# Performance work log

Measured on AMD Instinct MI355X. Metric: run time of the kernel, lower is better.

## Reference

```python
import jax, jax.numpy as jnp
import numpy as np

NT, NS, NH, NG, NR, NC = 365, 300, 128, 32, 8, 1


def _linear_params(key, fin, fout):
    k1, k2 = jax.random.split(key)
    s = 1.0 / np.sqrt(fin)
    W = jax.random.uniform(k1, (fout, fin), minval=-s, maxval=s, dtype=jnp.float32)
    b = jax.random.uniform(k2, (fout,), minval=-s, maxval=s, dtype=jnp.float32)
    return W, b


def setup_inputs() -> dict:
    key = jax.random.key(0)
    ks = jax.random.split(key, 9)
    x = jax.random.normal(ks[0], (NT, NS, 6), dtype=jnp.float32)
    xc = jax.random.normal(ks[1], (NS, NG), dtype=jnp.float32)
    fcR_w1, fcR_b1 = _linear_params(ks[2], NG, 256)
    fcR_w2, fcR_b2 = _linear_params(ks[3], 256, NH * NR)
    fcW_w1, fcW_b1 = _linear_params(ks[4], NG, 256)
    fcW_w2, fcW_b2 = _linear_params(ks[5], 256, NH * 7)
    fcT_w1, fcT_b1 = _linear_params(ks[6], 6 + NG, 256)
    fcT_w2, fcT_b2 = _linear_params(ks[7], 256, NH * 3)
    fcCT_w, fcCT_b = _linear_params(ks[8], 2 + NG, NC * NH * 3)
    return dict(x=x, xc=xc,
                fcR_w1=fcR_w1, fcR_b1=fcR_b1, fcR_w2=fcR_w2, fcR_b2=fcR_b2,
                fcW_w1=fcW_w1, fcW_b1=fcW_b1, fcW_w2=fcW_w2, fcW_b2=fcW_b2,
                fcT_w1=fcT_w1, fcT_b1=fcT_b1, fcT_w2=fcT_w2, fcT_b2=fcT_b2,
                fcCT_w=fcCT_w, fcCT_b=fcCT_b)


def _mlp(x, w1, b1, w2, b2):
    # Linear -> Tanh -> Dropout(identity in eval) -> Linear
    h = jnp.tanh(x @ w1.T + b1)
    return h @ w2.T + b2


def _conv_ts(q, r):
    # q: [nt, ns, nh]; r: [ns, nh, nr] routing weights. Causal temporal conv:
    # out[t] = sum_i q[t-i] * r[..., i]  (zero padded on the left)
    nt = q.shape[0]
    nr = r.shape[-1]
    qp = jnp.concatenate([jnp.zeros((nr - 1,) + q.shape[1:], q.dtype), q], axis=0)
    out = qp[nr - 1: nr - 1 + nt] * r[None, :, :, 0]
    for i in range(1, nr):
        out = out + qp[nr - 1 - i: nr - 1 - i + nt] * r[None, :, :, i]
    return out


def reference(x, xc, fcR_w1, fcR_b1, fcR_w2, fcR_b2,
              fcW_w1, fcW_b1, fcW_w2, fcW_b2,
              fcT_w1, fcT_b1, fcT_w2, fcT_b2,
              fcCT_w, fcCT_b):
    nh, nr = NH, NR
    P, E, T1, T2 = x[..., 0], x[..., 1], x[..., 2], x[..., 3]
    nt, ns = P.shape
    xcT = jnp.broadcast_to(xc[None], (nt, ns, xc.shape[-1]))
    xT = jnp.concatenate([x, xcT], axis=-1)                      # [nt, ns, 6+ng]

    # static gates per (site, bucket): sepPar with ['sigmoid']*4,'exp','relu','skip'
    w = _mlp(xc, fcW_w1, fcW_b1, fcW_w2, fcW_b2)                 # [ns, nh*7]
    kp = jax.nn.sigmoid(w[:, 0 * nh:1 * nh])
    ks_ = jax.nn.sigmoid(w[:, 1 * nh:2 * nh])
    kg = jax.nn.sigmoid(w[:, 2 * nh:3 * nh])
    gp = jax.nn.sigmoid(w[:, 3 * nh:4 * nh])
    gL = jnp.exp(w[:, 4 * nh:5 * nh]) * 2.0
    qb = jax.nn.relu(w[:, 5 * nh:6 * nh])
    ga = jax.nn.softmax(w[:, 6 * nh:7 * nh], axis=1)             # [ns, nh]

    # time-varying gates: ['skip','relu','exp']; vi overridden by hardsigmoid(v*2)
    v = _mlp(xT, fcT_w1, fcT_b1, fcT_w2, fcT_b2)                 # [nt, ns, nh*3]
    vi = jnp.clip(v[:, :, :nh] * 2.0 / 6.0 + 0.5, 0.0, 1.0)     # F.hardsigmoid(v*2)
    ve = jax.nn.relu(v[:, :, nh:2 * nh]) * 2.0
    vm = jnp.exp(v[:, :, 2 * nh:3 * nh])

    wR = _mlp(xc, fcR_w1, fcR_b1, fcR_w2, fcR_b2)                # [ns, nh*nr]
    r = jax.nn.relu(wR[:, :nh * nr]).reshape(ns, nh, nr)

    # snow fraction vf = arccos((T1+T2)/(T2-T1))/3.1415, overridden at extremes
    denom = T2 - T1
    ratio = jnp.clip((T1 + T2) / jnp.where(denom == 0, 1.0, denom), -1.0, 1.0)
    vf = jnp.arccos(ratio) / 3.1415
    vf = jnp.where(T1 >= 0, 0.0, jnp.where(T2 <= 0, 1.0, vf))
    Ps = P * vf                                                  # snow  [nt, ns]
    Pl = (P * (1.0 - vf))[:, :, None] * vi                       # rain  [nt, ns, nh]
    Ev = E[:, :, None] * ve                                      # evap  [nt, ns, nh]

    def step(carry, inp):
        Sf, Ss, Sg = carry
        Ps_k, Pl_k, Ev_k, vm_k = inp
        qf = jnp.minimum(Sf + Ps_k, vm_k)
        Sf = jax.nn.relu(Sf + Ps_k - vm_k)
        H = jax.nn.relu(Ss + Pl_k + qf - Ev_k)
        qp_ = jax.nn.relu(kp * (H - gL))
        qs = ks_ * jnp.minimum(H, gL)
        Ss = H - qp_ - qs
        qso = qs * (1.0 - gp)
        qsg = qs * gp
        qg = kg * (Sg + qsg) + qb
        Sg = (1.0 - kg) * (Sg + qsg) - qb
        return (Sf, Ss, Sg), (qp_, qso, qg)

    z = jnp.zeros((ns, nh), dtype=x.dtype)
    _, (Q1T, Q2T, Q3T) = jax.lax.scan(step, (z, z, z),
                                      (Ps[:, :, None], Pl, Ev, vm))

    Q1R = _conv_ts(Q1T, r)
    Q2R = _conv_ts(Q2T, r)
    Q3R = _conv_ts(Q3T, r)
    outQ = jnp.sum((Q1R + Q2R + Q3R) * ga, axis=2)               # [nt, ns]

    xTc = jnp.concatenate([T1[:, :, None], T2[:, :, None], xcT], axis=-1)
    wC = xTc @ fcCT_w.T + fcCT_b                                 # [nt, ns, nh*3]
    cp = jnp.exp(wC[:, :, 0 * nh:1 * nh])
    cs = jnp.exp(wC[:, :, 1 * nh:2 * nh])
    cg = jnp.exp(wC[:, :, 2 * nh:3 * nh])
    C1R = _conv_ts(Q1T * cp / 10.0, r)
    C2R = _conv_ts(Q2T * cs, r)
    C3R = _conv_ts(Q3T * cg, r)
    outC = jnp.sum((C1R + C2R + C3R) * ga, axis=2) / outQ
    return outQ, outC
```

## Files before the change

### kernel.cpp

```cpp
#include <hip/hip_runtime.h>
#include <math.h>

#define NTT 365
#define NSS 300
#define NROWS (NTT*NSS)
#define TPAD 384

using bf16x8 = __attribute__((ext_vector_type(8))) short;
using f32x4  = __attribute__((ext_vector_type(4))) float;

__device__ __forceinline__ float sigf(float v) { return 1.0f / (1.0f + __expf(-v)); }

__device__ __forceinline__ float tanhfast(float x) {
    float e = __expf(2.0f * x);
    return 1.0f - 2.0f * __builtin_amdgcn_rcpf(1.0f + e);
}

__device__ __forceinline__ unsigned short f2bf(float f) {
    unsigned u = __builtin_bit_cast(unsigned, f);
    u += 0x7FFFu + ((u >> 16) & 1u);
    return (unsigned short)(u >> 16);
}

__global__ __launch_bounds__(256) void k_prep(const float* __restrict__ w1,
                                              const float* __restrict__ w2,
                                              unsigned short* __restrict__ w1bf,
                                              unsigned short* __restrict__ w2bf)
{
    int idx = blockIdx.x * 256 + threadIdx.x;
    if (idx < 256 * 64) {
        int k = idx & 63;
        int r = idx >> 6;
        w1bf[idx] = (k < 38) ? f2bf(w1[r * 38 + k]) : (unsigned short)0;
    }
    int idx2 = idx - 256 * 64;
    if (idx2 >= 0 && idx2 < 384 * 256) w2bf[idx2] = f2bf(w2[idx2]);
}

__global__ __launch_bounds__(256) void k_site(
    const float* __restrict__ xc,
    const float* __restrict__ wW1, const float* __restrict__ bW1,
    const float* __restrict__ wW2, const float* __restrict__ bW2,
    const float* __restrict__ wR1, const float* __restrict__ bR1,
    const float* __restrict__ wR2, const float* __restrict__ bR2,
    float* __restrict__ wsite, float* __restrict__ rsite)
{
    __shared__ float xcb[10][32];
    __shared__ float hW[10][256];
    __shared__ float hR[10][256];
    int tid = threadIdx.x;
    int s0 = blockIdx.x * 10;
    int os = blockIdx.y;
    for (int i = tid; i < 10 * 32; i += 256) xcb[i / 32][i % 32] = xc[s0 * 32 + i];
    __syncthreads();
    {
        int j = tid;
        float aW[10], aR[10];
#pragma unroll
        for (int r = 0; r < 10; ++r) { aW[r] = bW1[j]; aR[r] = bR1[j]; }
        for (int k = 0; k < 32; ++k) {
            float wv = wW1[j * 32 + k], rv = wR1[j * 32 + k];
#pragma unroll
            for (int r = 0; r < 10; ++r) { float xv = xcb[r][k]; aW[r] += xv * wv; aR[r] += xv * rv; }
        }
#pragma unroll
        for (int r = 0; r < 10; ++r) { hW[r][j] = tanhfast(aW[r]); hR[r][j] = tanhfast(aR[r]); }
    }
    __syncthreads();
    if (tid < 240) {
        int o_lin = os * 240 + tid;
        float acc[10];
        if (o_lin < 896) {
            int o = o_lin;
#pragma unroll
            for (int r = 0; r < 10; ++r) acc[r] = bW2[o];
            for (int k = 0; k < 256; ++k) {
                float wv = wW2[o * 256 + k];
#pragma unroll
                for (int r = 0; r < 10; ++r) acc[r] += hW[r][k] * wv;
            }
#pragma unroll
            for (int r = 0; r < 10; ++r) wsite[(s0 + r) * 896 + o] = acc[r];
        } else {
            int o = o_lin - 896;
#pragma unroll
            for (int r = 0; r < 10; ++r) acc[r] = bR2[o];
            for (int k = 0; k < 256; ++k) {
                float wv = wR2[o * 256 + k];
#pragma unroll
                for (int r = 0; r < 10; ++r) acc[r] += hR[r][k] * wv;
            }
#pragma unroll
            for (int r = 0; r < 10; ++r) rsite[(s0 + r) * 1024 + o] = acc[r];
        }
    }
}

__global__ __launch_bounds__(128) void k_softmax_ga(const float* __restrict__ wsite,
                                                    float* __restrict__ ga)
{
    int s = blockIdx.x, tid = threadIdx.x;
    __shared__ float red[2];
    float v = wsite[s * 896 + 6 * 128 + tid];
    float m = v;
#pragma unroll
    for (int off = 32; off >= 1; off >>= 1) m = fmaxf(m, __shfl_xor(m, off));
    if ((tid & 63) == 0) red[tid >> 6] = m;
    __syncthreads();
    m = fmaxf(red[0], red[1]);
    __syncthreads();
    float e = __expf(v - m);
    float ssum = e;
#pragma unroll
    for (int off = 32; off >= 1; off >>= 1) ssum += __shfl_xor(ssum, off);
    if ((tid & 63) == 0) red[tid >> 6] = ssum;
    __syncthreads();
    ssum = red[0] + red[1];
    ga[s * 128 + tid] = e / ssum;
}

__global__ __launch_bounds__(512) void k_fcT(
    const float* __restrict__ x, const float* __restrict__ xc,
    const unsigned short* __restrict__ w1bf, const float* __restrict__ b1,
    const unsigned short* __restrict__ w2bf, const float* __restrict__ b2,
    float4* __restrict__ PT, float2* __restrict__ NV)
{
    __shared__ unsigned short A1[64][72];
    __shared__ unsigned short hb[64][264];
    __shared__ float2 pfE[64];
    int tid = threadIdx.x;
    int row0 = blockIdx.x * 64;

    for (int idx = tid; idx < 64 * 64; idx += 512) {
        int r = idx >> 6, c = idx & 63;
        int g = row0 + r;
        float val = 0.0f;
        if (g < NROWS) {
            if (c < 6) val = x[g * 6 + c];
            else if (c < 38) { int s = g % NSS; val = xc[s * 32 + (c - 6)]; }
        }
        A1[r][c] = f2bf(val);
    }
    if (tid < 64) {
        int r = tid, g = row0 + r;
        float P = 0, E = 0, T1 = 0, T2 = 0;
        if (g < NROWS) { P = x[g * 6]; E = x[g * 6 + 1]; T1 = x[g * 6 + 2]; T2 = x[g * 6 + 3]; }
        float den = T2 - T1;
        float dg = (den == 0.0f) ? 1.0f : den;
        float ratio = fminf(fmaxf((T1 + T2) / dg, -1.0f), 1.0f);
        float vf = acosf(ratio) * (1.0f / 3.1415f);
        vf = (T1 >= 0.0f) ? 0.0f : ((T2 <= 0.0f) ? 1.0f : vf);
        pfE[r] = make_float2(P * (1.0f - vf), 2.0f * E);
        if (g < NROWS) PT[g] = make_float4(P * vf, T1, T2, vf);
    }
    __syncthreads();

    int lane = tid & 63, wv = tid >> 6;
    int r16 = lane & 15;
    int kg = (lane >> 4) * 8;
    int rq = (lane >> 4) * 4;

    {
        int mt = wv & 3, nb = (wv >> 2) * 8;
        f32x4 acc[8];
#pragma unroll
        for (int i = 0; i < 8; ++i) acc[i] = (f32x4){0.f, 0.f, 0.f, 0.f};
#pragma unroll
        for (int ks = 0; ks < 2; ++ks) {
            bf16x8 a = *(const bf16x8*)&A1[mt * 16 + r16][ks * 32 + kg];
#pragma unroll
            for (int i = 0; i < 8; ++i) {
                bf16x8 b = *(const bf16x8*)(w1bf + ((nb + i) * 16 + r16) * 64 + ks * 32 + kg);
                acc[i] = __builtin_amdgcn_mfma_f32_16x16x32_bf16(a, b, acc[i], 0, 0, 0);
            }
        }
#pragma unroll
        for (int i = 0; i < 8; ++i) {
            int col = (nb + i) * 16 + r16;
            float bias = b1[col];
#pragma unroll
            for (int j = 0; j < 4; ++j) {
                int row = mt * 16 + rq + j;
                hb[row][col] = f2bf(tanhfast(acc[i][j] + bias));
            }
        }
    }
    __syncthreads();

    {
        int cb0 = wv * 16, cb1 = 128 + wv * 16, cb2 = 256 + wv * 16;
        f32x4 acc[4][3];
#pragma unroll
        for (int m = 0; m < 4; ++m)
#pragma unroll
            for (int c = 0; c < 3; ++c) acc[m][c] = (f32x4){0.f, 0.f, 0.f, 0.f};
#pragma unroll
        for (int ks = 0; ks < 8; ++ks) {
            bf16x8 b0 = *(const bf16x8*)(w2bf + (cb0 + r16) * 256 + ks * 32 + kg);
            bf16x8 b1v = *(const bf16x8*)(w2bf + (cb1 + r16) * 256 + ks * 32 + kg);
            bf16x8 b2v = *(const bf16x8*)(w2bf + (cb2 + r16) * 256 + ks * 32 + kg);
#pragma unroll
            for (int m = 0; m < 4; ++m) {
                bf16x8 a = *(const bf16x8*)&hb[m * 16 + r16][ks * 32 + kg];
                acc[m][0] = __builtin_amdgcn_mfma_f32_16x16x32_bf16(a, b0, acc[m][0], 0, 0, 0);
                acc[m][1] = __builtin_amdgcn_mfma_f32_16x16x32_bf16(a, b1v, acc[m][1], 0, 0, 0);
                acc[m][2] = __builtin_amdgcn_mfma_f32_16x16x32_bf16(a, b2v, acc[m][2], 0, 0, 0);
            }
        }
        int hcol = cb0 + r16;
        float bias0 = b2[cb0 + r16], bias1 = b2[cb1 + r16], bias2 = b2[cb2 + r16];
#pragma unroll
        for (int m = 0; m < 4; ++m) {
            float2 pf[4];
#pragma unroll
            for (int j = 0; j < 4; ++j) pf[j] = pfE[m * 16 + rq + j];
#pragma unroll
            for (int j = 0; j < 4; ++j) {
                int r = m * 16 + rq + j;
                int g = row0 + r;
                if (g < NROWS) {
                    float vi = fminf(fmaxf((acc[m][0][j] + bias0) * (1.0f / 3.0f) + 0.5f, 0.0f), 1.0f);
                    float pl = pf[j].x * vi;
                    float ev = pf[j].y * fmaxf(acc[m][1][j] + bias1, 0.0f);
                    float vmv = __expf(acc[m][2][j] + bias2);
                    NV[(size_t)g * 128 + hcol] = make_float2(pl - ev, vmv);
                }
            }
        }
    }
}

__global__ __launch_bounds__(64) void k_scan(
    const float* __restrict__ xc,
    const float* __restrict__ wsite, const float* __restrict__ rsite,
    const float* __restrict__ gaw,
    const float* __restrict__ ctw, const float* __restrict__ ctb,
    const float4* __restrict__ PTg, const float2* __restrict__ NV,
    float* __restrict__ pQ, float* __restrict__ pC)
{
    __shared__ float4 ptlds[TPAD];
    __shared__ __align__(16) float red[16][68];
    int lane = threadIdx.x;
    int b = blockIdx.x;
    int s = b >> 1, half = b & 1;
    int h = half * 64 + lane;

    for (int t = lane; t < TPAD; t += 64) ptlds[t] = PTg[(size_t)t * NSS + s];

    const float* wrow = wsite + s * 896;
    float kp = sigf(wrow[0 * 128 + h]);
    float ks = sigf(wrow[1 * 128 + h]);
    float kg = sigf(wrow[2 * 128 + h]);
    float gp = sigf(wrow[3 * 128 + h]);
    float gpc = 1.0f - gp;
    float gL = __expf(wrow[4 * 128 + h]) * 2.0f;
    float kpgl = kp * gL;
    float qb = fmaxf(wrow[5 * 128 + h], 0.0f);
    float ga = gaw[s * 128 + h];
    float rt0 = fmaxf(rsite[s * 1024 + h * 8 + 0], 0.0f) * ga;
    float rt1 = fmaxf(rsite[s * 1024 + h * 8 + 1], 0.0f) * ga;
    float rt2 = fmaxf(rsite[s * 1024 + h * 8 + 2], 0.0f) * ga;
    float rt3 = fmaxf(rsite[s * 1024 + h * 8 + 3], 0.0f) * ga;
    float rt4 = fmaxf(rsite[s * 1024 + h * 8 + 4], 0.0f) * ga;
    float rt5 = fmaxf(rsite[s * 1024 + h * 8 + 5], 0.0f) * ga;
    float rt6 = fmaxf(rsite[s * 1024 + h * 8 + 6], 0.0f) * ga;
    float rt7 = fmaxf(rsite[s * 1024 + h * 8 + 7], 0.0f) * ga;
    const float L2E = 1.4426950408889634f;
    const float LG01 = -3.3219280948873623f;
    float cpw0, cpw1, cpb, csw0, csw1, csb, cgw0, cgw1, cgb;
    {
        const float* wr = ctw + (0 * 128 + h) * 34;
        float base = ctb[0 * 128 + h];
        for (int k = 0; k < 32; ++k) base += wr[2 + k] * xc[s * 32 + k];
        cpw0 = wr[0] * L2E; cpw1 = wr[1] * L2E; cpb = base * L2E + LG01;
    }
    {
        const float* wr = ctw + (1 * 128 + h) * 34;
        float base = ctb[1 * 128 + h];
        for (int k = 0; k < 32; ++k) base += wr[2 + k] * xc[s * 32 + k];
        csw0 = wr[0] * L2E; csw1 = wr[1] * L2E; csb = base * L2E;
    }
    {
        const float* wr = ctw + (2 * 128 + h) * 34;
        float base = ctb[2 * 128 + h];
        for (int k = 0; k < 32; ++k) base += wr[2 + k] * xc[s * 32 + k];
        cgw0 = wr[0] * L2E; cgw1 = wr[1] * L2E; cgb = base * L2E;
    }
    float Sf = 0.0f, Ss = 0.0f, Sg = 0.0f;
    float q0 = 0, q1 = 0, q2 = 0, q3 = 0, q4 = 0, q5 = 0, q6 = 0, q7 = 0;
    float c0 = 0, c1 = 0, c2 = 0, c3 = 0, c4 = 0, c5 = 0, c6 = 0, c7 = 0;

    const float2* nvbase = NV + (size_t)s * 128 + h;
    float2 nv[16];
#pragma unroll
    for (int i = 0; i < 16; ++i) nv[i] = nvbase[(size_t)i * NSS * 128];

    float4 ptc = ptlds[0];
    float4 ptn = ptlds[1];

    auto reduce8 = [&](int base) {
        int v = lane >> 2, sub = lane & 3;
        const float4* rp = (const float4*)&red[v][0];
        float4 a0 = rp[sub * 4 + 0];
        float4 a1 = rp[sub * 4 + 1];
        float4 a2 = rp[sub * 4 + 2];
        float4 a3 = rp[sub * 4 + 3];
        float sA = (a0.x + a0.y) + (a0.z + a0.w);
        float sB = (a1.x + a1.y) + (a1.z + a1.w);
        float sC = (a2.x + a2.y) + (a2.z + a2.w);
        float sD = (a3.x + a3.y) + (a3.z + a3.w);
        float sm = (sA + sB) + (sC + sD);
        sm += __shfl_xor(sm, 1);
        sm += __shfl_xor(sm, 2);
        int t = base + (v & 7);
        if (sub == 0 && t < NTT) {
            float* bp = (v < 8) ? pQ : pC;
            bp[((size_t)t * NSS + s) * 2 + half] = sm;
        }
    };

    for (int tb = 0; tb < 368; tb += 16) {
#pragma unroll
        for (int u = 0; u < 16; ++u) {
            int t = tb + u;
            float net = nv[u].x, vm = nv[u].y;
            nv[u] = nvbase[(size_t)(t + 16) * NSS * 128];
            float psv = ptc.x, T1 = ptc.y, T2 = ptc.z;
            ptc = ptn;
            ptn = ptlds[t + 2];
            float t1v = Sf + psv;
            float qf = fminf(t1v, vm);
            Sf = fmaxf(t1v - vm, 0.0f);
            float H = fmaxf(Ss + qf + net, 0.0f);
            float qp = fmaxf(kp * H - kpgl, 0.0f);
            float qs = ks * fminf(H, gL);
            Ss = H - qp - qs;
            float qso = qs * gpc;
            float qsg = qs * gp;
            float tg = Sg + qsg;
            float qg = kg * tg + qb;
            Sg = tg - qg;
            float cp = exp2f(cpw0 * T1 + cpw1 * T2 + cpb);
            float cs = exp2f(csw0 * T1 + csw1 * T2 + csb);
            float cg = exp2f(cgw0 * T1 + cgw1 * T2 + cgb);
            float QS = qp + qso + qg;
            float CS = qp * cp + qso * cs + qg * cg;
            q0 += QS * rt0; q1 += QS * rt1; q2 += QS * rt2; q3 += QS * rt3;
            q4 += QS * rt4; q5 += QS * rt5; q6 += QS * rt6; q7 += QS * rt7;
            c0 += CS * rt0; c1 += CS * rt1; c2 += CS * rt2; c3 += CS * rt3;
            c4 += CS * rt4; c5 += CS * rt5; c6 += CS * rt6; c7 += CS * rt7;
            red[u & 7][lane] = q0;
            red[8 + (u & 7)][lane] = c0;
            q0 = q1; q1 = q2; q2 = q3; q3 = q4; q4 = q5; q5 = q6; q6 = q7; q7 = 0.0f;
            c0 = c1; c1 = c2; c2 = c3; c3 = c4; c4 = c5; c5 = c6; c6 = c7; c7 = 0.0f;
            if (u == 7) reduce8(tb);
            if (u == 15) reduce8(tb + 8);
        }
    }
}

__global__ __launch_bounds__(256) void k_final(const float* __restrict__ pQ,
                                               const float* __restrict__ pC,
                                               float* __restrict__ out)
{
    int i = blockIdx.x * 256 + threadIdx.x;
    if (i < NROWS) {
        float q = pQ[i * 2] + pQ[i * 2 + 1];
        float c = pC[i * 2] + pC[i * 2 + 1];
        out[i] = q;
        out[NROWS + i] = c / q;
    }
}

extern "C" void kernel_launch(void* const* d_in, const int* in_sizes, int n_in,
                              void* d_out, int out_size, void* d_ws, size_t ws_size,
                              hipStream_t stream)
{
    const float* x      = (const float*)d_in[0];
    const float* xc     = (const float*)d_in[1];
    const float* fcR_w1 = (const float*)d_in[2];
    const float* fcR_b1 = (const float*)d_in[3];
    const float* fcR_w2 = (const float*)d_in[4];
    const float* fcR_b2 = (const float*)d_in[5];
    const float* fcW_w1 = (const float*)d_in[6];
    const float* fcW_b1 = (const float*)d_in[7];
    const float* fcW_w2 = (const float*)d_in[8];
    const float* fcW_b2 = (const float*)d_in[9];
    const float* fcT_w1 = (const float*)d_in[10];
    const float* fcT_b1 = (const float*)d_in[11];
    const float* fcT_w2 = (const float*)d_in[12];
    const float* fcT_b2 = (const float*)d_in[13];
    const float* fcCT_w = (const float*)d_in[14];
    const float* fcCT_b = (const float*)d_in[15];
    float* out = (float*)d_out;

    float* ws = (float*)d_ws;
    size_t o_w    = 0;
    size_t o_r    = o_w  + 300 * 896;
    size_t o_ga   = o_r  + 300 * 1024;
    size_t o_PT   = o_ga + 300 * 128;
    size_t o_NV   = o_PT + (size_t)TPAD * NSS * 4;
    size_t o_pQ   = o_NV + (size_t)TPAD * NSS * 128 * 2;
    size_t o_pC   = o_pQ + (size_t)NROWS * 2;
    size_t o_w1bf = o_pC + (size_t)NROWS * 2;
    size_t o_w2bf = o_w1bf + 8192;

    float* wsite = ws + o_w;
    float* rsite = ws + o_r;
    float* gaw   = ws + o_ga;
    float4* PT   = (float4*)(ws + o_PT);
    float2* NV   = (float2*)(ws + o_NV);
    float* pQ    = ws + o_pQ;
    float* pC    = ws + o_pC;
    unsigned short* w1bf = (unsigned short*)(ws + o_w1bf);
    unsigned short* w2bf = (unsigned short*)(ws + o_w2bf);

    k_prep<<<448, 256, 0, stream>>>(fcT_w1, fcT_w2, w1bf, w2bf);
    k_site<<<dim3(30, 8), 256, 0, stream>>>(xc, fcW_w1, fcW_b1, fcW_w2, fcW_b2,
                                            fcR_w1, fcR_b1, fcR_w2, fcR_b2, wsite, rsite);
    k_softmax_ga<<<300, 128, 0, stream>>>(wsite, gaw);
    int nblk2 = (NROWS + 63) / 64;
    k_fcT<<<nblk2, 512, 0, stream>>>(x, xc, w1bf, fcT_b1, w2bf, fcT_b2, PT, NV);
    k_scan<<<600, 64, 0, stream>>>(xc, wsite, rsite, gaw, fcCT_w, fcCT_b,
                                   PT, NV, pQ, pC);
    k_final<<<(NROWS + 255) / 256, 256, 0, stream>>>(pQ, pC, out);
}
```

Measured before the change: 201.8 us.

## Pack NV intermediate as bf16 pairs and pre-swizzle MFMA weight fragments

The per-row NV intermediate (net input and vm) handed from the fcT kernel to the scan kernel is now stored as two packed bf16 values in one 32-bit word instead of a float2. This halves the global write and the serial scan's streaming read traffic. The fcT weights are also pre-arranged into per-lane MFMA fragment order, so each B-operand load becomes one contiguous 16-byte access. The scan deepens its PT prefetch ring from 2 to 4 entries. Storing vm and net in bf16 reduces precision in the recurrent state update, which risks accuracy drift over the 365-step scan.

```diff
diff --git a/kernel.cpp b/kernel.cpp
--- a/kernel.cpp
+++ b/kernel.cpp
@@ -24,17 +24,31 @@
 
 __global__ __launch_bounds__(256) void k_prep(const float* __restrict__ w1,
                                               const float* __restrict__ w2,
-                                              unsigned short* __restrict__ w1bf,
-                                              unsigned short* __restrict__ w2bf)
-{
-    int idx = blockIdx.x * 256 + threadIdx.x;
-    if (idx < 256 * 64) {
-        int k = idx & 63;
-        int r = idx >> 6;
-        w1bf[idx] = (k < 38) ? f2bf(w1[r * 38 + k]) : (unsigned short)0;
-    }
-    int idx2 = idx - 256 * 64;
-    if (idx2 >= 0 && idx2 < 384 * 256) w2bf[idx2] = f2bf(w2[idx2]);
+                                              unsigned short* __restrict__ w1s,
+                                              unsigned short* __restrict__ w2s)
+{
+    int G = blockIdx.x * 256 + threadIdx.x;
+    if (G < 2048) {
+        int lane = G & 63, ks = (G >> 6) & 1, tile = G >> 7;
+        int o = tile * 16 + (lane & 15);
+        int kb = ks * 32 + (lane >> 4) * 8;
+        unsigned short tmp[8];
+#pragma unroll
+        for (int e = 0; e < 8; ++e) {
+            int k = kb + e;
+            tmp[e] = (k < 38) ? f2bf(w1[o * 38 + k]) : (unsigned short)0;
+        }
+        *(bf16x8*)(w1s + (size_t)G * 8) = *(bf16x8*)tmp;
+    } else if (G < 2048 + 12288) {
+        int G2 = G - 2048;
+        int lane = G2 & 63, ks = (G2 >> 6) & 7, tile = G2 >> 9;
+        int o = tile * 16 + (lane & 15);
+        int kb = ks * 32 + (lane >> 4) * 8;
+        unsigned short tmp[8];
+#pragma unroll
+        for (int e = 0; e < 8; ++e) tmp[e] = f2bf(w2[o * 256 + kb + e]);
+        *(bf16x8*)(w2s + (size_t)G2 * 8) = *(bf16x8*)tmp;
+    }
 }
 
 __global__ __launch_bounds__(256) void k_site(
@@ -121,9 +135,9 @@
 
 __global__ __launch_bounds__(512) void k_fcT(
     const float* __restrict__ x, const float* __restrict__ xc,
-    const unsigned short* __restrict__ w1bf, const float* __restrict__ b1,
-    const unsigned short* __restrict__ w2bf, const float* __restrict__ b2,
-    float4* __restrict__ PT, float2* __restrict__ NV)
+    const unsigned short* __restrict__ w1s, const float* __restrict__ b1,
+    const unsigned short* __restrict__ w2s, const float* __restrict__ b2,
+    float4* __restrict__ PT, unsigned* __restrict__ NVu)
 {
     __shared__ unsigned short A1[64][72];
     __shared__ unsigned short hb[64][264];
@@ -170,7 +184,7 @@
             bf16x8 a = *(const bf16x8*)&A1[mt * 16 + r16][ks * 32 + kg];
 #pragma unroll
             for (int i = 0; i < 8; ++i) {
-                bf16x8 b = *(const bf16x8*)(w1bf + ((nb + i) * 16 + r16) * 64 + ks * 32 + kg);
+                bf16x8 b = *(const bf16x8*)(w1s + ((size_t)(((nb + i) * 2 + ks) * 64 + lane) << 3));
                 acc[i] = __builtin_amdgcn_mfma_f32_16x16x32_bf16(a, b, acc[i], 0, 0, 0);
             }
         }
@@ -188,7 +202,7 @@
     __syncthreads();
 
     {
-        int cb0 = wv * 16, cb1 = 128 + wv * 16, cb2 = 256 + wv * 16;
+        int t0 = wv, t1 = wv + 8, t2 = wv + 16;
         f32x4 acc[4][3];
 #pragma unroll
         for (int m = 0; m < 4; ++m)
@@ -196,9 +210,9 @@
             for (int c = 0; c < 3; ++c) acc[m][c] = (f32x4){0.f, 0.f, 0.f, 0.f};
 #pragma unroll
         for (int ks = 0; ks < 8; ++ks) {
-            bf16x8 b0 = *(const bf16x8*)(w2bf + (cb0 + r16) * 256 + ks * 32 + kg);
-            bf16x8 b1v = *(const bf16x8*)(w2bf + (cb1 + r16) * 256 + ks * 32 + kg);
-            bf16x8 b2v = *(const bf16x8*)(w2bf + (cb2 + r16) * 256 + ks * 32 + kg);
+            bf16x8 b0 = *(const bf16x8*)(w2s + ((size_t)((t0 * 8 + ks) * 64 + lane) << 3));
+            bf16x8 b1v = *(const bf16x8*)(w2s + ((size_t)((t1 * 8 + ks) * 64 + lane) << 3));
+            bf16x8 b2v = *(const bf16x8*)(w2s + ((size_t)((t2 * 8 + ks) * 64 + lane) << 3));
 #pragma unroll
             for (int m = 0; m < 4; ++m) {
                 bf16x8 a = *(const bf16x8*)&hb[m * 16 + r16][ks * 32 + kg];
@@ -207,8 +221,8 @@
                 acc[m][2] = __builtin_amdgcn_mfma_f32_16x16x32_bf16(a, b2v, acc[m][2], 0, 0, 0);
             }
         }
-        int hcol = cb0 + r16;
-        float bias0 = b2[cb0 + r16], bias1 = b2[cb1 + r16], bias2 = b2[cb2 + r16];
+        int hcol = wv * 16 + r16;
+        float bias0 = b2[hcol], bias1 = b2[128 + hcol], bias2 = b2[256 + hcol];
 #pragma unroll
         for (int m = 0; m < 4; ++m) {
             float2 pf[4];
@@ -223,7 +237,8 @@
                     float pl = pf[j].x * vi;
                     float ev = pf[j].y * fmaxf(acc[m][1][j] + bias1, 0.0f);
                     float vmv = __expf(acc[m][2][j] + bias2);
-                    NV[(size_t)g * 128 + hcol] = make_float2(pl - ev, vmv);
+                    unsigned pk = (unsigned)f2bf(pl - ev) | ((unsigned)f2bf(vmv) << 16);
+                    NVu[(size_t)g * 128 + hcol] = pk;
                 }
             }
         }
@@ -235,7 +250,7 @@
     const float* __restrict__ wsite, const float* __restrict__ rsite,
     const float* __restrict__ gaw,
     const float* __restrict__ ctw, const float* __restrict__ ctb,
-    const float4* __restrict__ PTg, const float2* __restrict__ NV,
+    const float4* __restrict__ PTg, const unsigned* __restrict__ NVu,
     float* __restrict__ pQ, float* __restrict__ pC)
 {
     __shared__ float4 ptlds[TPAD];
@@ -290,13 +305,14 @@
     float q0 = 0, q1 = 0, q2 = 0, q3 = 0, q4 = 0, q5 = 0, q6 = 0, q7 = 0;
     float c0 = 0, c1 = 0, c2 = 0, c3 = 0, c4 = 0, c5 = 0, c6 = 0, c7 = 0;
 
-    const float2* nvbase = NV + (size_t)s * 128 + h;
-    float2 nv[16];
+    const unsigned* nvbase = NVu + (size_t)s * 128 + h;
+    unsigned nv[16];
 #pragma unroll
     for (int i = 0; i < 16; ++i) nv[i] = nvbase[(size_t)i * NSS * 128];
 
-    float4 ptc = ptlds[0];
-    float4 ptn = ptlds[1];
+    float4 pt[4];
+#pragma unroll
+    for (int i = 0; i < 4; ++i) pt[i] = ptlds[i];
 
     auto reduce8 = [&](int base) {
         int v = lane >> 2, sub = lane & 3;
@@ -323,11 +339,12 @@
 #pragma unroll
         for (int u = 0; u < 16; ++u) {
             int t = tb + u;
-            float net = nv[u].x, vm = nv[u].y;
+            unsigned nvu = nv[u];
+            float net = __builtin_bit_cast(float, nvu << 16);
+            float vm  = __builtin_bit_cast(float, nvu & 0xFFFF0000u);
             nv[u] = nvbase[(size_t)(t + 16) * NSS * 128];
-            float psv = ptc.x, T1 = ptc.y, T2 = ptc.z;
-            ptc = ptn;
-            ptn = ptlds[t + 2];
+            float psv = pt[u & 3].x, T1 = pt[u & 3].y, T2 = pt[u & 3].z;
+            pt[u & 3] = ptlds[t + 4];
             float t1v = Sf + psv;
             float qf = fminf(t1v, vm);
             Sf = fmaxf(t1v - vm, 0.0f);
@@ -400,7 +417,7 @@
     size_t o_ga   = o_r  + 300 * 1024;
     size_t o_PT   = o_ga + 300 * 128;
     size_t o_NV   = o_PT + (size_t)TPAD * NSS * 4;
-    size_t o_pQ   = o_NV + (size_t)TPAD * NSS * 128 * 2;
+    size_t o_pQ   = o_NV + (size_t)TPAD * NSS * 128;
     size_t o_pC   = o_pQ + (size_t)NROWS * 2;
     size_t o_w1bf = o_pC + (size_t)NROWS * 2;
     size_t o_w2bf = o_w1bf + 8192;
@@ -409,19 +426,19 @@
     float* rsite = ws + o_r;
     float* gaw   = ws + o_ga;
     float4* PT   = (float4*)(ws + o_PT);
-    float2* NV   = (float2*)(ws + o_NV);
+    unsigned* NVu = (unsigned*)(ws + o_NV);
     float* pQ    = ws + o_pQ;
     float* pC    = ws + o_pC;
-    unsigned short* w1bf = (unsigned short*)(ws + o_w1bf);
-    unsigned short* w2bf = (unsigned short*)(ws + o_w2bf);
-
-    k_prep<<<448, 256, 0, stream>>>(fcT_w1, fcT_w2, w1bf, w2bf);
+    unsigned short* w1s = (unsigned short*)(ws + o_w1bf);
+    unsigned short* w2s = (unsigned short*)(ws + o_w2bf);
+
+    k_prep<<<56, 256, 0, stream>>>(fcT_w1, fcT_w2, w1s, w2s);
     k_site<<<dim3(30, 8), 256, 0, stream>>>(xc, fcW_w1, fcW_b1, fcW_w2, fcW_b2,
                                             fcR_w1, fcR_b1, fcR_w2, fcR_b2, wsite, rsite);
     k_softmax_ga<<<300, 128, 0, stream>>>(wsite, gaw);
     int nblk2 = (NROWS + 63) / 64;
-    k_fcT<<<nblk2, 512, 0, stream>>>(x, xc, w1bf, fcT_b1, w2bf, fcT_b2, PT, NV);
+    k_fcT<<<nblk2, 512, 0, stream>>>(x, xc, w1s, fcT_b1, w2s, fcT_b2, PT, NVu);
     k_scan<<<600, 64, 0, stream>>>(xc, wsite, rsite, gaw, fcCT_w, fcCT_b,
-                                   PT, NV, pQ, pC);
+                                   PT, NVu, pQ, pC);
     k_final<<<(NROWS + 255) / 256, 256, 0, stream>>>(pQ, pC, out);
 }
```

Result: faster. 161.5 us (-20.0%).
